# Kernel tuning notes

Measured on AMD Instinct MI355X. Metric: run time of the kernel, lower is better.

Reference implementation:

```python
import jax, jax.numpy as jnp
import numpy as np

N_HEAD = 8
N_FEAT = 512
D_HEAD = N_FEAT // N_HEAD


def setup_inputs() -> dict:
    key = jax.random.key(0)
    ks = jax.random.split(key, 11)
    B, T, L = 4, 2048, 16
    s = 1.0 / np.sqrt(D_HEAD)
    so = 1.0 / np.sqrt(N_FEAT)
    return {
        "q": jax.random.normal(ks[0], (B, T, 1, N_FEAT), jnp.float32),
        "k": jax.random.normal(ks[1], (B, T, L, N_FEAT), jnp.float32),
        "v": jax.random.normal(ks[2], (B, T, L, N_FEAT), jnp.float32),
        "Wq": jax.random.uniform(ks[3], (D_HEAD, D_HEAD), jnp.float32, -s, s),
        "bq": jax.random.uniform(ks[4], (D_HEAD,), jnp.float32, -s, s),
        "Wk": jax.random.uniform(ks[5], (D_HEAD, D_HEAD), jnp.float32, -s, s),
        "bk": jax.random.uniform(ks[6], (D_HEAD,), jnp.float32, -s, s),
        "Wv": jax.random.uniform(ks[7], (D_HEAD, D_HEAD), jnp.float32, -s, s),
        "bv": jax.random.uniform(ks[8], (D_HEAD,), jnp.float32, -s, s),
        "Wo": jax.random.uniform(ks[9], (N_FEAT, N_FEAT), jnp.float32, -so, so),
        "bo": jax.random.uniform(ks[10], (N_FEAT,), jnp.float32, -so, so),
    }


def reference(q, k, v, Wq, bq, Wk, bk, Wv, bv, Wo, bo):
    B, T, L, F = k.shape
    H, D = N_HEAD, D_HEAD
    # split heads: q [B,T,H,D] (query axis of length 1 squeezed), k/v [B,T,L,H,D]
    qh = q.reshape(B, T, H, D)
    kh = k.reshape(B, T, L, H, D)
    vh = v.reshape(B, T, L, H, D)
    # per-head linear projections (shared across heads), Linear: x @ W^T + b
    qh = jnp.einsum("bthd,ed->bthe", qh, Wq) + bq
    kh = jnp.einsum("btlhd,ed->btlhe", kh, Wk) + bk
    vh = jnp.einsum("btlhd,ed->btlhe", vh, Wv) + bv
    # attention scores over the local window L (query length 1 per timestep)
    attw = jnp.einsum("bthd,btlhd->bthl", qh, kh) / jnp.sqrt(jnp.asarray(D, qh.dtype))
    attn = jax.nn.softmax(attw, axis=-1)  # dropout is identity in eval mode
    ct = jnp.einsum("bthl,btlhd->bthd", attn, vh)
    ct = ct.reshape(B, T, F)
    return ct @ Wo.T + bo
```

## Files before the change

### kernel.cpp

```cpp
#include <hip/hip_runtime.h>


#define NFEAT 512
#define NHEAD 8
#define DHEAD 64
#define LWIN  16
#define NBT   32
#define VPITCH 520

typedef __attribute__((ext_vector_type(8))) short bf16x8;
typedef __attribute__((ext_vector_type(4))) float f32x4;

__device__ __forceinline__ unsigned short f2bf(float f) {
    unsigned int u = __float_as_uint(f);
    unsigned int r = (u + 0x7fffu + ((u >> 16) & 1u)) >> 16;
    return (unsigned short)r;
}

__device__ __forceinline__ void gload16(const float* src, float* dst) {
    __builtin_amdgcn_global_load_lds((const __attribute__((address_space(1))) float*)src,
                                     (__attribute__((address_space(3))) float*)dst,
                                     16, 0, 0);
}
__device__ __forceinline__ void gload4(const float* src, float* dst) {
    __builtin_amdgcn_global_load_lds((const __attribute__((address_space(1))) float*)src,
                                     (__attribute__((address_space(3))) float*)dst,
                                     4, 0, 0);
}

__global__ void precompute_small(const float* __restrict__ Wq, const float* __restrict__ bq,
                                 const float* __restrict__ Wk,
                                 const float* __restrict__ Wo, const float* __restrict__ bo,
                                 const float* __restrict__ bv,
                                 float* __restrict__ A, float* __restrict__ g,
                                 float* __restrict__ b2) {
    int idx = blockIdx.x * 256 + threadIdx.x;
    if (idx < 4096) {
        int d = idx >> 6, dp = idx & 63;
        float s = 0.f;
        #pragma unroll 8
        for (int e = 0; e < 64; ++e) s = fmaf(Wq[e * 64 + d], Wk[e * 64 + dp], s);
        A[idx] = s;
    } else if (idx < 4160) {
        int dp = idx - 4096;
        float s = 0.f;
        #pragma unroll 8
        for (int e = 0; e < 64; ++e) s = fmaf(Wk[e * 64 + dp], bq[e], s);
        g[dp] = s;
    } else if (idx < 4672) {
        int j = idx - 4160;
        float s = bo[j];
        #pragma unroll 8
        for (int i = 0; i < 512; ++i) s = fmaf(Wo[j * 512 + i], bv[i & 63], s);
        b2[j] = s;
    }
}

__global__ void precompute_wo2(const float* __restrict__ Wo, const float* __restrict__ Wv,
                               unsigned short* __restrict__ Wo2B) {
    int idx = blockIdx.x * 256 + threadIdx.x;
    int i = idx & 511, j = idx >> 9;
    int h = i >> 6, e = i & 63;
    float s = 0.f;
    #pragma unroll 8
    for (int d = 0; d < 64; ++d)
        s = fmaf(Wo[j * 512 + h * 64 + d], Wv[d * 64 + e], s);
    Wo2B[(size_t)j * 512 + i] = f2bf(s);
}

__global__ __launch_bounds__(512, 1)
void attn_mono(const float* __restrict__ q, const float* __restrict__ k,
               const float* __restrict__ v, const float* __restrict__ A,
               const float* __restrict__ g, const unsigned short* __restrict__ Wo2B,
               const float* __restrict__ b2, float* __restrict__ out) {
    __shared__ __align__(16) float kbuf[2][LWIN][NFEAT];
    __shared__ __align__(16) float vbuf[2][LWIN][NFEAT];
    __shared__ __align__(16) float qbuf[2][NFEAT];
    __shared__ __align__(16) float wmbuf[NFEAT];
    __shared__ __align__(16) unsigned short vbarS[16 * VPITCH];

    const int tid  = threadIdx.x;
    const int w    = tid >> 6;
    const int lane = tid & 63;
    const int lq   = lane >> 2;
    const int d4   = lane & 3;
    const int bt0  = blockIdx.x * NBT;

    float Areg[64];
    #pragma unroll
    for (int d = 0; d < 64; ++d) Areg[d] = A[d * 64 + lane];
    const float greg = g[lane];

    #define ISSUE_TILE(buf, bti)                                                  \
    {                                                                             \
        const float* kb_ = k + (size_t)(bti) * (LWIN * NFEAT);                    \
        const float* vb_ = v + (size_t)(bti) * (LWIN * NFEAT);                    \
        _Pragma("unroll")                                                         \
        for (int rr = 0; rr < 2; ++rr) {                                          \
            const int r_    = 2 * w + rr;                                         \
            const int kofs_ = ((lane * 16) ^ ((r_ & 7) << 4)) >> 2;               \
            gload16(kb_ + r_ * NFEAT +       kofs_,     &kbuf[buf][r_][0]);       \
            gload16(kb_ + r_ * NFEAT + 256 + kofs_,     &kbuf[buf][r_][256]);     \
            gload16(vb_ + r_ * NFEAT +       lane * 4,  &vbuf[buf][r_][0]);       \
            gload16(vb_ + r_ * NFEAT + 256 + lane * 4,  &vbuf[buf][r_][256]);     \
        }                                                                         \
        gload4(q + (size_t)(bti) * NFEAT + w * 64 + lane, &qbuf[buf][w * 64]);    \
    }

    ISSUE_TILE(0, bt0 + 0);
    ISSUE_TILE(1, bt0 + 1);

    const int half  = (w >> 2) & 1;
    const int hwoff = (w & 3) * 256 + d4 * 64;
    const int swz   = (lq & 7) << 4;

    for (int i = 0; i < NBT; ++i) {
        const int cur = i & 1;
        const int bt  = bt0 + i;

        if (i + 1 < NBT) {
            asm volatile("s_waitcnt vmcnt(9)" ::: "memory");
        } else {
            asm volatile("s_waitcnt vmcnt(0)" ::: "memory");
        }
        __builtin_amdgcn_sched_barrier(0);
        __builtin_amdgcn_s_barrier();
        __builtin_amdgcn_sched_barrier(0);

        {
            const float* qrow = &qbuf[cur][w * 64];
            float c0 = 0.f, c1 = 0.f, c2 = 0.f, c3 = 0.f;
            #pragma unroll
            for (int d = 0; d < 64; d += 4) {
                c0 = fmaf(qrow[d + 0], Areg[d + 0], c0);
                c1 = fmaf(qrow[d + 1], Areg[d + 1], c1);
                c2 = fmaf(qrow[d + 2], Areg[d + 2], c2);
                c3 = fmaf(qrow[d + 3], Areg[d + 3], c3);
            }
            wmbuf[w * 64 + lane] = (greg + (c0 + c1) + (c2 + c3)) * 0.125f;
        }
        asm volatile("s_waitcnt lgkmcnt(0)" ::: "memory");
        __builtin_amdgcn_sched_barrier(0);

        const float* wmp = &wmbuf[w * 64 + d4 * 16];
        const float4 wm0 = *(const float4*)(wmp + 0);
        const float4 wm1 = *(const float4*)(wmp + 4);
        const float4 wm2 = *(const float4*)(wmp + 8);
        const float4 wm3 = *(const float4*)(wmp + 12);

        const char* rowb = (const char*)&kbuf[cur][lq][0] + half * 1024;
        const float4 k0 = *(const float4*)(rowb + ((hwoff +  0) ^ swz));
        const float4 k1 = *(const float4*)(rowb + ((hwoff + 16) ^ swz));
        const float4 k2 = *(const float4*)(rowb + ((hwoff + 32) ^ swz));
        const float4 k3 = *(const float4*)(rowb + ((hwoff + 48) ^ swz));
        float s0 = wm0.x * k0.x, s1 = wm1.x * k1.x, s2 = wm2.x * k2.x, s3 = wm3.x * k3.x;
        s0 = fmaf(wm0.y, k0.y, s0); s1 = fmaf(wm1.y, k1.y, s1);
        s2 = fmaf(wm2.y, k2.y, s2); s3 = fmaf(wm3.y, k3.y, s3);
        s0 = fmaf(wm0.z, k0.z, s0); s1 = fmaf(wm1.z, k1.z, s1);
        s2 = fmaf(wm2.z, k2.z, s2); s3 = fmaf(wm3.z, k3.z, s3);
        s0 = fmaf(wm0.w, k0.w, s0); s1 = fmaf(wm1.w, k1.w, s1);
        s2 = fmaf(wm2.w, k2.w, s2); s3 = fmaf(wm3.w, k3.w, s3);
        float s = (s0 + s1) + (s2 + s3);
        s += __shfl_xor(s, 1, 64);
        s += __shfl_xor(s, 2, 64);
        const float e = __expf(s);

        float den = 0.f, accv = 0.f;
        #pragma unroll
        for (int l = 0; l < LWIN; ++l) {
            const float el = __shfl(e, 4 * l, 64);
            den += el;
            accv = fmaf(el, vbuf[cur][l][w * 64 + lane], accv);
        }
        vbarS[(i & 15) * VPITCH + w * 64 + lane] = f2bf(accv * (1.0f / den));

        asm volatile("s_waitcnt lgkmcnt(0)" ::: "memory");
        __builtin_amdgcn_sched_barrier(0);
        __builtin_amdgcn_s_barrier();
        __builtin_amdgcn_sched_barrier(0);

        if (i + 2 < NBT) {
            ISSUE_TILE(cur, bt + 2);
        }
        __builtin_amdgcn_sched_barrier(0);

        if ((i & 15) == 15) {
            const int m0   = bt - 15;
            const int n0   = w * 64;
            const int r    = lane & 15;
            const int kg   = lane >> 4;

            const unsigned short* As0 = vbarS + r * VPITCH + kg * 8;
            const short* Bb0 = (const short*)Wo2B + ((size_t)(n0 +  0 + r)) * 512 + kg * 8;
            const short* Bb1 = (const short*)Wo2B + ((size_t)(n0 + 16 + r)) * 512 + kg * 8;
            const short* Bb2 = (const short*)Wo2B + ((size_t)(n0 + 32 + r)) * 512 + kg * 8;
            const short* Bb3 = (const short*)Wo2B + ((size_t)(n0 + 48 + r)) * 512 + kg * 8;

            f32x4 acc0 = {0.f, 0.f, 0.f, 0.f}, acc1 = acc0, acc2 = acc0, acc3 = acc0;
            #pragma unroll 4
            for (int kk = 0; kk < 16; ++kk) {
                const bf16x8 a   = *reinterpret_cast<const bf16x8*>(As0 + kk * 32);
                const bf16x8 b0  = *reinterpret_cast<const bf16x8*>(Bb0 + kk * 32);
                const bf16x8 b1  = *reinterpret_cast<const bf16x8*>(Bb1 + kk * 32);
                const bf16x8 b2v = *reinterpret_cast<const bf16x8*>(Bb2 + kk * 32);
                const bf16x8 b3  = *reinterpret_cast<const bf16x8*>(Bb3 + kk * 32);
                acc0 = __builtin_amdgcn_mfma_f32_16x16x32_bf16(a, b0,  acc0, 0, 0, 0);
                acc1 = __builtin_amdgcn_mfma_f32_16x16x32_bf16(a, b1,  acc1, 0, 0, 0);
                acc2 = __builtin_amdgcn_mfma_f32_16x16x32_bf16(a, b2v, acc2, 0, 0, 0);
                acc3 = __builtin_amdgcn_mfma_f32_16x16x32_bf16(a, b3,  acc3, 0, 0, 0);
            }

            const float bb0 = b2[n0 + 0 + r],  bb1 = b2[n0 + 16 + r];
            const float bb2 = b2[n0 + 32 + r], bb3 = b2[n0 + 48 + r];
            #pragma unroll
            for (int j = 0; j < 4; ++j) {
                const size_t row = (size_t)(m0 + kg * 4 + j) * 512;
                out[row + n0 +  0 + r] = acc0[j] + bb0;
                out[row + n0 + 16 + r] = acc1[j] + bb1;
                out[row + n0 + 32 + r] = acc2[j] + bb2;
                out[row + n0 + 48 + r] = acc3[j] + bb3;
            }
        }
    }
    #undef ISSUE_TILE
}

extern "C" void kernel_launch(void* const* d_in, const int* in_sizes, int n_in,
                              void* d_out, int out_size, void* d_ws, size_t ws_size,
                              hipStream_t stream) {
    const float* q  = (const float*)d_in[0];
    const float* k  = (const float*)d_in[1];
    const float* v  = (const float*)d_in[2];
    const float* Wq = (const float*)d_in[3];
    const float* bq = (const float*)d_in[4];
    const float* Wk = (const float*)d_in[5];
    const float* Wv = (const float*)d_in[7];
    const float* bv = (const float*)d_in[8];
    const float* Wo = (const float*)d_in[9];
    const float* bo = (const float*)d_in[10];
    float* out = (float*)d_out;

    float* ws = (float*)d_ws;
    float*          A    = ws;
    float*          g    = ws + 4096;
    float*          b2   = ws + 4160;
    unsigned short* Wo2B = (unsigned short*)(ws + 4672);

    const int BT = in_sizes[0] / NFEAT;

    hipLaunchKernelGGL(precompute_small, dim3(19), dim3(256), 0, stream,
                       Wq, bq, Wk, Wo, bo, bv, A, g, b2);
    hipLaunchKernelGGL(precompute_wo2, dim3(1024), dim3(256), 0, stream,
                       Wo, Wv, Wo2B);
    hipLaunchKernelGGL(attn_mono, dim3(BT / NBT), dim3(512), 0, stream,
                       q, k, v, A, g, Wo2B, b2, out);
}
```

Measured before the change: 179.0 us.

## Prefetch q two tiles ahead and compute next query weights before barrier

Moves the per-timestep q·A weight computation for tile i+1 ahead of the block barrier of tile i. To make the data available, q loads are issued two tiles ahead into a 4-slot buffer and wm is double-buffered. This takes the q projection and its LDS round trip off the critical path after each barrier. In exchange it uses more LDS and needs more intricate vmcnt accounting, which may be fragile.

```diff
diff --git a/kernel.cpp b/kernel.cpp
--- a/kernel.cpp
+++ b/kernel.cpp
@@ -75,8 +75,8 @@
                const float* __restrict__ b2, float* __restrict__ out) {
     __shared__ __align__(16) float kbuf[2][LWIN][NFEAT];
     __shared__ __align__(16) float vbuf[2][LWIN][NFEAT];
-    __shared__ __align__(16) float qbuf[2][NFEAT];
-    __shared__ __align__(16) float wmbuf[NFEAT];
+    __shared__ __align__(16) float qbuf[4][NFEAT];
+    __shared__ __align__(16) float wmbuf[2][NFEAT];
     __shared__ __align__(16) unsigned short vbarS[16 * VPITCH];
 
     const int tid  = threadIdx.x;
@@ -104,11 +104,34 @@
             gload16(vb_ + r_ * NFEAT +       lane * 4,  &vbuf[buf][r_][0]);       \
             gload16(vb_ + r_ * NFEAT + 256 + lane * 4,  &vbuf[buf][r_][256]);     \
         }                                                                         \
-        gload4(q + (size_t)(bti) * NFEAT + w * 64 + lane, &qbuf[buf][w * 64]);    \
-    }
-
+        int qbt_ = (bti) + 2;                                                     \
+        if (qbt_ > bt0 + NBT - 1) qbt_ = bt0 + NBT - 1;                           \
+        gload4(q + (size_t)qbt_ * NFEAT + w * 64 + lane,                          \
+               &qbuf[(qbt_ - bt0) & 3][w * 64]);                                  \
+    }
+
+    #define COMPUTE_W(qslot, wslot)                                               \
+    {                                                                             \
+        const float* qrow_ = &qbuf[qslot][w * 64];                                \
+        float c0_ = 0.f, c1_ = 0.f, c2_ = 0.f, c3_ = 0.f;                         \
+        _Pragma("unroll")                                                         \
+        for (int d = 0; d < 64; d += 4) {                                         \
+            const float4 qv_ = *(const float4*)(qrow_ + d);                       \
+            c0_ = fmaf(qv_.x, Areg[d + 0], c0_);                                  \
+            c1_ = fmaf(qv_.y, Areg[d + 1], c1_);                                  \
+            c2_ = fmaf(qv_.z, Areg[d + 2], c2_);                                  \
+            c3_ = fmaf(qv_.w, Areg[d + 3], c3_);                                  \
+        }                                                                         \
+        wmbuf[wslot][w * 64 + lane] = (greg + (c0_ + c1_) + (c2_ + c3_)) * 0.125f;\
+    }
+
+    gload4(q + (size_t)(bt0 + 0) * NFEAT + w * 64 + lane, &qbuf[0][w * 64]);
+    gload4(q + (size_t)(bt0 + 1) * NFEAT + w * 64 + lane, &qbuf[1][w * 64]);
     ISSUE_TILE(0, bt0 + 0);
     ISSUE_TILE(1, bt0 + 1);
+    asm volatile("s_waitcnt vmcnt(18)" ::: "memory");
+    __builtin_amdgcn_sched_barrier(0);
+    COMPUTE_W(0, 0);
 
     const int half  = (w >> 2) & 1;
     const int hwoff = (w & 3) * 256 + d4 * 64;
@@ -117,6 +140,11 @@
     for (int i = 0; i < NBT; ++i) {
         const int cur = i & 1;
         const int bt  = bt0 + i;
+
+        if (i + 1 < NBT) {
+            COMPUTE_W((i + 1) & 3, (i + 1) & 1);
+        }
+        __builtin_amdgcn_sched_barrier(0);
 
         if (i + 1 < NBT) {
             asm volatile("s_waitcnt vmcnt(9)" ::: "memory");
@@ -127,22 +155,7 @@
         __builtin_amdgcn_s_barrier();
         __builtin_amdgcn_sched_barrier(0);
 
-        {
-            const float* qrow = &qbuf[cur][w * 64];
-            float c0 = 0.f, c1 = 0.f, c2 = 0.f, c3 = 0.f;
-            #pragma unroll
-            for (int d = 0; d < 64; d += 4) {
-                c0 = fmaf(qrow[d + 0], Areg[d + 0], c0);
-                c1 = fmaf(qrow[d + 1], Areg[d + 1], c1);
-                c2 = fmaf(qrow[d + 2], Areg[d + 2], c2);
-                c3 = fmaf(qrow[d + 3], Areg[d + 3], c3);
-            }
-            wmbuf[w * 64 + lane] = (greg + (c0 + c1) + (c2 + c3)) * 0.125f;
-        }
-        asm volatile("s_waitcnt lgkmcnt(0)" ::: "memory");
-        __builtin_amdgcn_sched_barrier(0);
-
-        const float* wmp = &wmbuf[w * 64 + d4 * 16];
+        const float* wmp = &wmbuf[i & 1][w * 64 + d4 * 16];
         const float4 wm0 = *(const float4*)(wmp + 0);
         const float4 wm1 = *(const float4*)(wmp + 4);
         const float4 wm2 = *(const float4*)(wmp + 8);
@@ -223,6 +236,7 @@
         }
     }
     #undef ISSUE_TILE
+    #undef COMPUTE_W
 }
 
 extern "C" void kernel_launch(void* const* d_in, const int* in_sizes, int n_in,
```

After: 180.0 us. No clear change (+0.6%).
